# Kernel tuning notes

Measured on AMD Instinct MI355X. Metric: run time of the kernel, lower is better.

## Reference

```python
import jax, jax.numpy as jnp
import numpy as np

COEFF = 0.97  # de-emphasis coefficient (module init kwarg)


def setup_inputs() -> dict:
    key = jax.random.key(0)
    waveform = jax.random.normal(key, (32, 2, 480000), dtype=jnp.float32)
    return {"waveform": waveform}


def reference(waveform) -> jnp.ndarray:
    # y[n] = x[n] + COEFF * y[n-1] along the last axis.
    # Expressed as a first-order linear recurrence y_n = a_n*y_{n-1} + b_n
    # with a_n = COEFF (constant), b_n = x[n], solved with a log-depth
    # associative scan: (a1,b1) o (a2,b2) = (a1*a2, a2*b1 + b2).
    a = jnp.full_like(waveform, COEFF)

    def combine(left, right):
        a_l, b_l = left
        a_r, b_r = right
        return (a_l * a_r, a_r * b_l + b_r)

    _, y = jax.lax.associative_scan(combine, (a, waveform), axis=-1)
    return y
```

## Files before the change

kernel.cpp:

```cpp
#include <hip/hip_runtime.h>


#define COEFF 0.97f
#define ROW_LEN 480000
#define SEG 16
#define BLOCK 256
#define HALO 512
#define SPAN (BLOCK * SEG)
#define OUT_PER_BLOCK (SPAN - HALO)
#define BLOCKS_PER_ROW ((ROW_LEN + OUT_PER_BLOCK - 1) / OUT_PER_BLOCK)
#define CHUNKS (SPAN / 4)
#define HALO_CHUNKS (HALO / 4)
#define CPT (SEG / 4)
#define K_ITERS (CHUNKS / BLOCK)

typedef float v4f __attribute__((ext_vector_type(4)));

constexpr float fpow(float b, int n) {
    float r = 1.0f;
    for (int i = 0; i < n; ++i) r *= b;
    return r;
}
constexpr float CSEG      = fpow(COEFF, SEG);
constexpr float CWAVESPAN = fpow(COEFF, 64 * SEG);

struct Pows { float p[SEG + 1]; };
constexpr Pows make_pows() {
    Pows P{};
    float r = 1.0f;
    for (int i = 0; i <= SEG; ++i) { P.p[i] = r; r *= COEFF; }
    return P;
}
constexpr Pows PW = make_pows();

__device__ __forceinline__ int swz(int m) {
    const int o = m >> 2, c = m & 3;
    return (o << 2) | (c ^ ((o >> 1) & 3));
}

__global__ __launch_bounds__(BLOCK) void deemph_kernel(const float* __restrict__ x,
                                                       float* __restrict__ y) {
    __shared__ v4f lds[CHUNKS];
    __shared__ float wsum[BLOCK / 64];

    const int row  = blockIdx.y;
    const int blk  = blockIdx.x;
    const int t    = threadIdx.x;
    const int lane = t & 63;
    const int wave = t >> 6;

    const long long row_base = (long long)row * ROW_LEN;
    const int span_start = blk * OUT_PER_BLOCK - HALO;

    #pragma unroll
    for (int k = 0; k < K_ITERS; ++k) {
        const int m = t + k * BLOCK;
        const int e = span_start + 4 * m;
        v4f v = {0.0f, 0.0f, 0.0f, 0.0f};
        if (e >= 0 && e < ROW_LEN)
            v = *(const v4f*)(x + row_base + e);
        lds[swz(m)] = v;
    }
    __syncthreads();

    float l[SEG];
    #pragma unroll
    for (int c = 0; c < CPT; ++c) {
        v4f v = lds[swz(t * CPT + c)];
        l[4*c+0] = v.x; l[4*c+1] = v.y; l[4*c+2] = v.z; l[4*c+3] = v.w;
    }

    #pragma unroll
    for (int i = 1; i < SEG; ++i) l[i] = fmaf(COEFF, l[i-1], l[i]);

    float A = CSEG;
    float B = l[SEG-1];
    #pragma unroll
    for (int d = 1; d < 64; d <<= 1) {
        float Ap = __shfl_up(A, d);
        float Bp = __shfl_up(B, d);
        if (lane >= d) { B = fmaf(A, Bp, B); A *= Ap; }
    }
    float Aex = __shfl_up(A, 1);
    float Bex = __shfl_up(B, 1);
    if (lane == 0) { Aex = 1.0f; Bex = 0.0f; }

    if (lane == 63) wsum[wave] = B;
    __syncthreads();
    float Cw = 0.0f;
    #pragma unroll
    for (int v = 0; v < BLOCK / 64 - 1; ++v)
        if (v < wave) Cw = fmaf(CWAVESPAN, Cw, wsum[v]);

    const float K = fmaf(Aex, Cw, Bex);

    #pragma unroll
    for (int i = 0; i < SEG; ++i) l[i] = fmaf(K, PW.p[i + 1], l[i]);

    #pragma unroll
    for (int c = 0; c < CPT; ++c) {
        v4f v;
        v.x = l[4*c+0]; v.y = l[4*c+1]; v.z = l[4*c+2]; v.w = l[4*c+3];
        lds[swz(t * CPT + c)] = v;
    }
    __syncthreads();

    #pragma unroll
    for (int k = 0; k < K_ITERS; ++k) {
        const int m = t + k * BLOCK;
        const int e = span_start + 4 * m;
        if (m >= HALO_CHUNKS && e < ROW_LEN)
            *(v4f*)(y + row_base + e) = lds[swz(m)];
    }
}

extern "C" void kernel_launch(void* const* d_in, const int* in_sizes, int n_in,
                              void* d_out, int out_size, void* d_ws, size_t ws_size,
                              hipStream_t stream) {
    (void)n_in; (void)d_ws; (void)ws_size; (void)out_size;
    const float* x = (const float*)d_in[0];
    float* y = (float*)d_out;
    const int n_rows = in_sizes[0] / ROW_LEN;
    dim3 grid(BLOCKS_PER_ROW, n_rows);
    deemph_kernel<<<grid, BLOCK, 0, stream>>>(x, y);
}
```

Baseline: 215.5 us.

## Process multiple tiles per block with double-buffered direct-to-LDS loads and carry

Each block now walks 8 tiles of a row and carries the recurrence state between tiles, so the 512-sample halo is recomputed once per 8 tiles instead of once per tile. The next tile is prefetched into a second LDS buffer with global_load_lds while the current one is computed. Segment length drops to 8 and the wave-scan decay factors become constants, which shortens the shuffle scan. In exchange the kernel relies on hand-placed waitcnt and barrier instructions, launches far fewer blocks, and each block runs a serial chain of tiles.

```diff
diff --git a/kernel.cpp b/kernel.cpp
--- a/kernel.cpp
+++ b/kernel.cpp
@@ -3,14 +3,15 @@
 
 #define COEFF 0.97f
 #define ROW_LEN 480000
-#define SEG 16
+#define SEG 8
 #define BLOCK 256
+#define WAVES (BLOCK / 64)
 #define HALO 512
 #define SPAN (BLOCK * SEG)
-#define OUT_PER_BLOCK (SPAN - HALO)
+#define TILES 8
+#define OUT_PER_BLOCK (TILES * SPAN - HALO)
 #define BLOCKS_PER_ROW ((ROW_LEN + OUT_PER_BLOCK - 1) / OUT_PER_BLOCK)
 #define CHUNKS (SPAN / 4)
-#define HALO_CHUNKS (HALO / 4)
 #define CPT (SEG / 4)
 #define K_ITERS (CHUNKS / BLOCK)
 
@@ -21,8 +22,14 @@
     for (int i = 0; i < n; ++i) r *= b;
     return r;
 }
-constexpr float CSEG      = fpow(COEFF, SEG);
-constexpr float CWAVESPAN = fpow(COEFF, 64 * SEG);
+constexpr float CSEG  = fpow(COEFF, SEG);
+constexpr float CWAVE = fpow(COEFF, 64 * SEG);
+constexpr float WF0 = fpow(COEFF, SEG * 1);
+constexpr float WF1 = fpow(COEFF, SEG * 2);
+constexpr float WF2 = fpow(COEFF, SEG * 4);
+constexpr float WF3 = fpow(COEFF, SEG * 8);
+constexpr float WF4 = fpow(COEFF, SEG * 16);
+constexpr float WF5 = fpow(COEFF, SEG * 32);
 
 struct Pows { float p[SEG + 1]; };
 constexpr Pows make_pows() {
@@ -33,15 +40,41 @@
 }
 constexpr Pows PW = make_pows();
 
-__device__ __forceinline__ int swz(int m) {
-    const int o = m >> 2, c = m & 3;
-    return (o << 2) | (c ^ ((o >> 1) & 3));
+__device__ __forceinline__ int swz(int m) { return m ^ ((m >> 3) & 1); }
+
+#define GLOAD_LDS(gp, lp)                                                     \
+    __builtin_amdgcn_global_load_lds(                                         \
+        (const __attribute__((address_space(1))) void*)(gp),                  \
+        (__attribute__((address_space(3))) void*)(lp), 16, 0, 0)
+
+__device__ __forceinline__ void stage_tile(const float* __restrict__ xrow,
+                                           v4f* dstbuf, int tbase,
+                                           int t, int wave) {
+    if (tbase >= 0 && tbase + SPAN <= ROW_LEN) {
+        #pragma unroll
+        for (int k = 0; k < K_ITERS; ++k) {
+            const int p  = k * BLOCK + t;
+            const int gc = swz(p);
+            v4f* dst = dstbuf + (k * BLOCK + (wave << 6));
+            GLOAD_LDS(xrow + tbase + 4 * gc, dst);
+        }
+    } else {
+        #pragma unroll
+        for (int k = 0; k < K_ITERS; ++k) {
+            const int p  = k * BLOCK + t;
+            const int gc = swz(p);
+            const int e  = tbase + 4 * gc;
+            v4f v = {0.0f, 0.0f, 0.0f, 0.0f};
+            if (e >= 0 && e < ROW_LEN) v = *(const v4f*)(xrow + e);
+            dstbuf[p] = v;
+        }
+    }
 }
 
 __global__ __launch_bounds__(BLOCK) void deemph_kernel(const float* __restrict__ x,
                                                        float* __restrict__ y) {
-    __shared__ v4f lds[CHUNKS];
-    __shared__ float wsum[BLOCK / 64];
+    __shared__ v4f buf[2][CHUNKS];
+    __shared__ float ws[WAVES];
 
     const int row  = blockIdx.y;
     const int blk  = blockIdx.x;
@@ -49,68 +82,96 @@
     const int lane = t & 63;
     const int wave = t >> 6;
 
-    const long long row_base = (long long)row * ROW_LEN;
+    const float* __restrict__ xrow = x + (long long)row * ROW_LEN;
+    float* __restrict__ yrow       = y + (long long)row * ROW_LEN;
+
     const int span_start = blk * OUT_PER_BLOCK - HALO;
+    const int out_lo     = blk * OUT_PER_BLOCK;
+
+    float Aex = 1.0f;
+    if (lane & 1)  Aex *= WF0;
+    if (lane & 2)  Aex *= WF1;
+    if (lane & 4)  Aex *= WF2;
+    if (lane & 8)  Aex *= WF3;
+    if (lane & 16) Aex *= WF4;
+    if (lane & 32) Aex *= WF5;
+
+    stage_tile(xrow, &buf[0][0], span_start, t, wave);
+    asm volatile("s_waitcnt vmcnt(0) lgkmcnt(0)" ::: "memory");
+
+    float CB = 0.0f;
 
     #pragma unroll
-    for (int k = 0; k < K_ITERS; ++k) {
-        const int m = t + k * BLOCK;
-        const int e = span_start + 4 * m;
-        v4f v = {0.0f, 0.0f, 0.0f, 0.0f};
-        if (e >= 0 && e < ROW_LEN)
-            v = *(const v4f*)(x + row_base + e);
-        lds[swz(m)] = v;
-    }
-    __syncthreads();
+    for (int tt = 0; tt < TILES; ++tt) {
+        const int cur = tt & 1;
+        const int tile_base = span_start + tt * SPAN;
 
-    float l[SEG];
-    #pragma unroll
-    for (int c = 0; c < CPT; ++c) {
-        v4f v = lds[swz(t * CPT + c)];
-        l[4*c+0] = v.x; l[4*c+1] = v.y; l[4*c+2] = v.z; l[4*c+3] = v.w;
-    }
+        __builtin_amdgcn_s_barrier();
+        asm volatile("" ::: "memory");
 
-    #pragma unroll
-    for (int i = 1; i < SEG; ++i) l[i] = fmaf(COEFF, l[i-1], l[i]);
+        if (tt + 1 < TILES)
+            stage_tile(xrow, &buf[cur ^ 1][0], tile_base + SPAN, t, wave);
 
-    float A = CSEG;
-    float B = l[SEG-1];
-    #pragma unroll
-    for (int d = 1; d < 64; d <<= 1) {
-        float Ap = __shfl_up(A, d);
-        float Bp = __shfl_up(B, d);
-        if (lane >= d) { B = fmaf(A, Bp, B); A *= Ap; }
-    }
-    float Aex = __shfl_up(A, 1);
-    float Bex = __shfl_up(B, 1);
-    if (lane == 0) { Aex = 1.0f; Bex = 0.0f; }
+        float l[SEG];
+        #pragma unroll
+        for (int c = 0; c < CPT; ++c) {
+            v4f v = buf[cur][swz(CPT * t + c)];
+            l[4*c+0] = v.x; l[4*c+1] = v.y; l[4*c+2] = v.z; l[4*c+3] = v.w;
+        }
+        #pragma unroll
+        for (int i = 1; i < SEG; ++i) l[i] = fmaf(COEFF, l[i-1], l[i]);
 
-    if (lane == 63) wsum[wave] = B;
-    __syncthreads();
-    float Cw = 0.0f;
-    #pragma unroll
-    for (int v = 0; v < BLOCK / 64 - 1; ++v)
-        if (v < wave) Cw = fmaf(CWAVESPAN, Cw, wsum[v]);
+        float Bv = l[SEG-1];
+        {
+            float Bp;
+            Bp = __shfl_up(Bv, 1);  if (lane >= 1)  Bv = fmaf(WF0, Bp, Bv);
+            Bp = __shfl_up(Bv, 2);  if (lane >= 2)  Bv = fmaf(WF1, Bp, Bv);
+            Bp = __shfl_up(Bv, 4);  if (lane >= 4)  Bv = fmaf(WF2, Bp, Bv);
+            Bp = __shfl_up(Bv, 8);  if (lane >= 8)  Bv = fmaf(WF3, Bp, Bv);
+            Bp = __shfl_up(Bv, 16); if (lane >= 16) Bv = fmaf(WF4, Bp, Bv);
+            Bp = __shfl_up(Bv, 32); if (lane >= 32) Bv = fmaf(WF5, Bp, Bv);
+        }
+        float Bex = __shfl_up(Bv, 1);
+        if (lane == 0) Bex = 0.0f;
+        if (lane == 63) ws[wave] = Bv;
 
-    const float K = fmaf(Aex, Cw, Bex);
+        asm volatile("s_waitcnt lgkmcnt(0)" ::: "memory");
+        __builtin_amdgcn_s_barrier();
+        asm volatile("" ::: "memory");
 
-    #pragma unroll
-    for (int i = 0; i < SEG; ++i) l[i] = fmaf(K, PW.p[i + 1], l[i]);
+        float Cw = CB;
+        #pragma unroll
+        for (int v = 0; v < WAVES - 1; ++v)
+            if (v < wave) Cw = fmaf(CWAVE, Cw, ws[v]);
+        const float K = fmaf(Aex, Cw, Bex);
+        #pragma unroll
+        for (int i = 0; i < SEG; ++i) l[i] = fmaf(K, PW.p[i + 1], l[i]);
 
-    #pragma unroll
-    for (int c = 0; c < CPT; ++c) {
-        v4f v;
-        v.x = l[4*c+0]; v.y = l[4*c+1]; v.z = l[4*c+2]; v.w = l[4*c+3];
-        lds[swz(t * CPT + c)] = v;
-    }
-    __syncthreads();
+        #pragma unroll
+        for (int v = 0; v < WAVES; ++v) CB = fmaf(CWAVE, CB, ws[v]);
 
-    #pragma unroll
-    for (int k = 0; k < K_ITERS; ++k) {
-        const int m = t + k * BLOCK;
-        const int e = span_start + 4 * m;
-        if (m >= HALO_CHUNKS && e < ROW_LEN)
-            *(v4f*)(y + row_base + e) = lds[swz(m)];
+        #pragma unroll
+        for (int c = 0; c < CPT; ++c) {
+            v4f v;
+            v.x = l[4*c+0]; v.y = l[4*c+1]; v.z = l[4*c+2]; v.w = l[4*c+3];
+            buf[cur][swz(CPT * t + c)] = v;
+        }
+
+        asm volatile("s_waitcnt lgkmcnt(0)" ::: "memory");
+        __builtin_amdgcn_s_barrier();
+        asm volatile("" ::: "memory");
+
+        #pragma unroll
+        for (int k = 0; k < K_ITERS; ++k) {
+            const int p = k * BLOCK + t;
+            const int e = tile_base + 4 * swz(p);
+            v4f v = buf[cur][p];
+            if (e >= out_lo && e < ROW_LEN)
+                *(v4f*)(yrow + e) = v;
+        }
+
+        if (tt + 1 < TILES)
+            asm volatile("s_waitcnt vmcnt(2)" ::: "memory");
     }
 }
 
```

Result: slower. 220.2 us (+2.2%).

## Replace block-level LDS scan with per-wave sequential chunked scan and prefetch

Applied to the files above, without the earlier changes.

Each wave now independently processes a strip of 16 output chunks of 256 samples plus a 512-sample halo. It walks the chunks sequentially with a wave-level shuffle scan and carries the running state across chunks, instead of staging a whole block tile in LDS with barriers. Loads are software-prefetched three chunks ahead in registers. This removes LDS traffic and block-wide syncs, at the cost of a serial per-chunk shuffle dependency chain within each wave.

```diff
diff --git a/kernel.cpp b/kernel.cpp
--- a/kernel.cpp
+++ b/kernel.cpp
@@ -3,16 +3,16 @@
 
 #define COEFF 0.97f
 #define ROW_LEN 480000
-#define SEG 16
+#define HALO 512
+#define SPAN_W 256
+#define P_HALO (HALO / SPAN_W)
+#define P_OUT 16
+#define P_TOT (P_OUT + P_HALO)
+#define OUT_W (P_OUT * SPAN_W)
+#define WPR ((ROW_LEN + OUT_W - 1) / OUT_W)
 #define BLOCK 256
-#define HALO 512
-#define SPAN (BLOCK * SEG)
-#define OUT_PER_BLOCK (SPAN - HALO)
-#define BLOCKS_PER_ROW ((ROW_LEN + OUT_PER_BLOCK - 1) / OUT_PER_BLOCK)
-#define CHUNKS (SPAN / 4)
-#define HALO_CHUNKS (HALO / 4)
-#define CPT (SEG / 4)
-#define K_ITERS (CHUNKS / BLOCK)
+#define WAVES (BLOCK / 64)
+#define PF 3
 
 typedef float v4f __attribute__((ext_vector_type(4)));
 
@@ -21,96 +21,89 @@
     for (int i = 0; i < n; ++i) r *= b;
     return r;
 }
-constexpr float CSEG      = fpow(COEFF, SEG);
-constexpr float CWAVESPAN = fpow(COEFF, 64 * SEG);
+constexpr float W4   = fpow(COEFF, 4);
+constexpr float W8   = fpow(COEFF, 8);
+constexpr float W16  = fpow(COEFF, 16);
+constexpr float W32  = fpow(COEFF, 32);
+constexpr float W64  = fpow(COEFF, 64);
+constexpr float W128 = fpow(COEFF, 128);
+constexpr float W256 = fpow(COEFF, 256);
+constexpr float C1P  = fpow(COEFF, 1);
+constexpr float C2P  = fpow(COEFF, 2);
+constexpr float C3P  = fpow(COEFF, 3);
+constexpr float C4P  = fpow(COEFF, 4);
 
-struct Pows { float p[SEG + 1]; };
-constexpr Pows make_pows() {
-    Pows P{};
-    float r = 1.0f;
-    for (int i = 0; i <= SEG; ++i) { P.p[i] = r; r *= COEFF; }
-    return P;
-}
-constexpr Pows PW = make_pows();
+__global__ __launch_bounds__(BLOCK, 8) void deemph_kernel(const float* __restrict__ x,
+                                                          float* __restrict__ y) {
+    const int lane = threadIdx.x & 63;
+    const int wave = threadIdx.x >> 6;
+    const int widx = blockIdx.x * WAVES + wave;
+    if (widx >= WPR) return;
+    const int row  = blockIdx.y;
 
-__device__ __forceinline__ int swz(int m) {
-    const int o = m >> 2, c = m & 3;
-    return (o << 2) | (c ^ ((o >> 1) & 3));
-}
+    const float* __restrict__ xrow = x + (long long)row * ROW_LEN;
+    float* __restrict__ yrow       = y + (long long)row * ROW_LEN;
 
-__global__ __launch_bounds__(BLOCK) void deemph_kernel(const float* __restrict__ x,
-                                                       float* __restrict__ y) {
-    __shared__ v4f lds[CHUNKS];
-    __shared__ float wsum[BLOCK / 64];
+    const int le = widx * OUT_W - HALO + 4 * lane;
 
-    const int row  = blockIdx.y;
-    const int blk  = blockIdx.x;
-    const int t    = threadIdx.x;
-    const int lane = t & 63;
-    const int wave = t >> 6;
+    float Aex = 1.0f;
+    if (lane & 1)  Aex *= W4;
+    if (lane & 2)  Aex *= W8;
+    if (lane & 4)  Aex *= W16;
+    if (lane & 8)  Aex *= W32;
+    if (lane & 16) Aex *= W64;
+    if (lane & 32) Aex *= W128;
 
-    const long long row_base = (long long)row * ROW_LEN;
-    const int span_start = blk * OUT_PER_BLOCK - HALO;
-
+    v4f r[PF];
     #pragma unroll
-    for (int k = 0; k < K_ITERS; ++k) {
-        const int m = t + k * BLOCK;
-        const int e = span_start + 4 * m;
+    for (int p = 0; p < PF; ++p) {
+        const int e = le + p * SPAN_W;
         v4f v = {0.0f, 0.0f, 0.0f, 0.0f};
-        if (e >= 0 && e < ROW_LEN)
-            v = *(const v4f*)(x + row_base + e);
-        lds[swz(m)] = v;
-    }
-    __syncthreads();
-
-    float l[SEG];
-    #pragma unroll
-    for (int c = 0; c < CPT; ++c) {
-        v4f v = lds[swz(t * CPT + c)];
-        l[4*c+0] = v.x; l[4*c+1] = v.y; l[4*c+2] = v.z; l[4*c+3] = v.w;
+        if (e >= 0 && e < ROW_LEN) v = *(const v4f*)(xrow + e);
+        r[p] = v;
     }
 
+    float c = 0.0f;
     #pragma unroll
-    for (int i = 1; i < SEG; ++i) l[i] = fmaf(COEFF, l[i-1], l[i]);
+    for (int p = 0; p < P_TOT; ++p) {
+        v4f v = r[p % PF];
+        if (p + PF < P_TOT) {
+            const int e2 = le + (p + PF) * SPAN_W;
+            v4f nv = {0.0f, 0.0f, 0.0f, 0.0f};
+            if (e2 >= 0 && e2 < ROW_LEN) nv = *(const v4f*)(xrow + e2);
+            r[p % PF] = nv;
+        }
 
-    float A = CSEG;
-    float B = l[SEG-1];
-    #pragma unroll
-    for (int d = 1; d < 64; d <<= 1) {
-        float Ap = __shfl_up(A, d);
-        float Bp = __shfl_up(B, d);
-        if (lane >= d) { B = fmaf(A, Bp, B); A *= Ap; }
-    }
-    float Aex = __shfl_up(A, 1);
-    float Bex = __shfl_up(B, 1);
-    if (lane == 0) { Aex = 1.0f; Bex = 0.0f; }
+        const float l0 = v.x;
+        const float l1 = fmaf(COEFF, l0, v.y);
+        const float l2 = fmaf(COEFF, l1, v.z);
+        const float l3 = fmaf(COEFF, l2, v.w);
 
-    if (lane == 63) wsum[wave] = B;
-    __syncthreads();
-    float Cw = 0.0f;
-    #pragma unroll
-    for (int v = 0; v < BLOCK / 64 - 1; ++v)
-        if (v < wave) Cw = fmaf(CWAVESPAN, Cw, wsum[v]);
+        float Bv = l3, Bp;
+        Bp = __shfl_up(Bv, 1);  if (lane >= 1)  Bv = fmaf(W4,   Bp, Bv);
+        Bp = __shfl_up(Bv, 2);  if (lane >= 2)  Bv = fmaf(W8,   Bp, Bv);
+        Bp = __shfl_up(Bv, 4);  if (lane >= 4)  Bv = fmaf(W16,  Bp, Bv);
+        Bp = __shfl_up(Bv, 8);  if (lane >= 8)  Bv = fmaf(W32,  Bp, Bv);
+        Bp = __shfl_up(Bv, 16); if (lane >= 16) Bv = fmaf(W64,  Bp, Bv);
+        Bp = __shfl_up(Bv, 32); if (lane >= 32) Bv = fmaf(W128, Bp, Bv);
+        float Bex = __shfl_up(Bv, 1);
+        if (lane == 0) Bex = 0.0f;
+        const float B63 = __shfl(Bv, 63);
 
-    const float K = fmaf(Aex, Cw, Bex);
+        const float Kt = fmaf(c, Aex, Bex);
+        c = fmaf(c, W256, B63);
 
-    #pragma unroll
-    for (int i = 0; i < SEG; ++i) l[i] = fmaf(K, PW.p[i + 1], l[i]);
-
-    #pragma unroll
-    for (int c = 0; c < CPT; ++c) {
-        v4f v;
-        v.x = l[4*c+0]; v.y = l[4*c+1]; v.z = l[4*c+2]; v.w = l[4*c+3];
-        lds[swz(t * CPT + c)] = v;
-    }
-    __syncthreads();
-
-    #pragma unroll
-    for (int k = 0; k < K_ITERS; ++k) {
-        const int m = t + k * BLOCK;
-        const int e = span_start + 4 * m;
-        if (m >= HALO_CHUNKS && e < ROW_LEN)
-            *(v4f*)(y + row_base + e) = lds[swz(m)];
+        if (p >= P_HALO) {
+            const int e = le + p * SPAN_W;
+            if (e < ROW_LEN) {
+                v4f o;
+                o.x = fmaf(Kt, C1P, l0);
+                o.y = fmaf(Kt, C2P, l1);
+                o.z = fmaf(Kt, C3P, l2);
+                o.w = fmaf(Kt, C4P, l3);
+                *(v4f*)(yrow + e) = o;
+            }
+        }
     }
 }
 
@@ -121,6 +114,6 @@
     const float* x = (const float*)d_in[0];
     float* y = (float*)d_out;
     const int n_rows = in_sizes[0] / ROW_LEN;
-    dim3 grid(BLOCKS_PER_ROW, n_rows);
+    dim3 grid((WPR + WAVES - 1) / WAVES, n_rows);
     deemph_kernel<<<grid, BLOCK, 0, stream>>>(x, y);
 }
```

New measurement: 217.4 us. No clear change (+0.9%).
